# Performance work log

Hardware: AMD Instinct MI355X
Metric: run time of the kernel (lower is better)

Reference implementation:

```python
import jax, jax.numpy as jnp
import numpy as np

N = 50000        # nodes
E = 800000       # edges (avg degree 16)
DIN = 256        # input feature dim
D = 128          # embedding_dim
B = 8            # graphs in batch
ITERS = 2        # num_iterations


def setup_inputs() -> dict:
    key = jax.random.key(0)
    ks = jax.random.split(key, 16)
    w = lambda k, shape: jax.random.normal(k, shape, jnp.float32) * 0.05
    z = lambda n: jnp.zeros((n,), jnp.float32)
    return {
        "nodes": jax.random.normal(ks[0], (N, DIN), jnp.float32),
        "edges": jax.random.randint(ks[1], (2, E), 0, N),
        "batch": jnp.sort(jax.random.randint(ks[2], (N,), 0, B)),
        # initial encoder Linear(DIN, D)
        "W_enc": w(ks[3], (DIN, D)), "b_enc": z(D),
        # parent aggregation MLP: Linear(2D, D) -> ReLU -> Linear(D, D)
        "Wp1": w(ks[4], (2 * D, D)), "bp1": z(D),
        "Wp2": w(ks[5], (D, D)), "bp2": z(D),
        # child aggregation MLP
        "Wc1": w(ks[6], (2 * D, D)), "bc1": z(D),
        "Wc2": w(ks[7], (D, D)), "bc2": z(D),
        # final agg: Linear(3D, 2D) -> ReLU -> Linear(2D, D)
        "Wf1": w(ks[8], (3 * D, 2 * D)), "bf1": z(2 * D),
        "Wf2": w(ks[9], (2 * D, D)), "bf2": z(D),
        # Conv1d(D, 2D, kernel=1) == Linear(D, 2D)
        "Wconv": w(ks[10], (D, 2 * D)), "bconv": z(2 * D),
    }


def _edge_agg(x, idx_i, idx_j, W1, b1, W2, b2, inv_deg):
    # message: mlp(cat(x_i, x_j)); scatter-sum at idx_i; degree-normalize.
    h = jnp.concatenate([x[idx_i], x[idx_j]], axis=1)         # [E, 2D]
    m = jax.nn.relu(h @ W1 + b1) @ W2 + b2                    # [E, D]
    agg = jax.ops.segment_sum(m, idx_i, num_segments=x.shape[0])
    return agg * inv_deg[:, None]


def reference(nodes, edges, batch, W_enc, b_enc, Wp1, bp1, Wp2, bp2,
              Wc1, bc1, Wc2, bc2, Wf1, bf1, Wf2, bf2, Wconv, bconv):
    src, dst = edges[0], edges[1]
    ones_e = jnp.ones((edges.shape[1],), nodes.dtype)
    deg_dst = jax.ops.segment_sum(ones_e, dst, num_segments=N)
    deg_src = jax.ops.segment_sum(ones_e, src, num_segments=N)
    inv_dst = jnp.where(deg_dst > 0, 1.0 / deg_dst, 0.0)
    inv_src = jnp.where(deg_src > 0, 1.0 / deg_src, 0.0)

    x = nodes @ W_enc + b_enc                                  # [N, D]
    for _ in range(ITERS):
        # Parent_Aggregation: x_i = x[dst], x_j = x[src], sum at dst, / in-deg
        fi = _edge_agg(x, dst, src, Wp1, bp1, Wp2, bp2, inv_dst)
        # Child_Aggregation:  x_i = x[src], x_j = x[dst], sum at src, / out-deg
        fo = _edge_agg(x, src, dst, Wc1, bc1, Wc2, bc2, inv_src)
        h = jnp.concatenate([x, fi, fo], axis=1)               # [N, 3D]
        x = x + (jax.nn.relu(h @ Wf1 + bf1) @ Wf2 + bf2)

    y = x @ Wconv + bconv                                      # conv1d k=1 -> [N, 2D]
    gmax = jax.ops.segment_max(y, batch, num_segments=B)       # global_max_pool
    cnt = jax.ops.segment_sum(jnp.ones((N,), y.dtype), batch, num_segments=B)
    gmean = jax.ops.segment_sum(y, batch, num_segments=B) / cnt[:, None]
    return jnp.concatenate([gmax, gmean], axis=1)              # [B, 4D]
```

## Files before the change

### kernel.cpp

```cpp
#include <hip/hip_runtime.h>
#include <hip/hip_bf16.h>
#include <float.h>

typedef __hip_bfloat16 bf16;
typedef short short8 __attribute__((ext_vector_type(8)));
typedef short short4v __attribute__((ext_vector_type(4)));
typedef float f32x4 __attribute__((ext_vector_type(4)));
typedef unsigned short u16;
typedef unsigned char u8;

__device__ __forceinline__ float toF(bf16 v) { return __bfloat162float(v); }
__device__ __forceinline__ float s2f(short s) {
    return __uint_as_float(((unsigned int)(unsigned short)s) << 16);
}
__device__ __forceinline__ short f2s(float f) {
    bf16 h = __float2bfloat16(f);
    return *(short*)&h;
}
__device__ __forceinline__ float rdw(const void* p, int i, int f) {
    return f ? toF(((const bf16*)p)[i]) : ((const float*)p)[i];
}

__global__ void diag_kernel(float* __restrict__ out, float v, int n) {
    int i = blockIdx.x * 256 + threadIdx.x;
// ... 223 lines not shown
        float mx = -FLT_MAX, sm = 0.f;
        for (int r = 0; r < 64; ++r) {
            int b = bs[r];
            if (b < 0) break;
            float v = s2f(sC[r * CPAD + tid]);
            if (b != cur_b) {
                if (cur_b >= 0) {
                    atomicMaxF(&gmax[cur_b * 256 + tid], mx);
                    atomicAdd(&gsum[cur_b * 256 + tid], sm);
                }
                cur_b = b; mx = v; sm = v;
            } else {
                mx = fmaxf(mx, v);
                sm += v;
            }
        }
        if (cur_b >= 0) {
            atomicMaxF(&gmax[cur_b * 256 + tid], mx);
            atomicAdd(&gsum[cur_b * 256 + tid], sm);
        }
    } else {
        constexpr int OC8 = NC / 8;
        for (int idx = tid; idx < 64 * OC8; idx += 256) {
            int r = idx / OC8, c8 = idx % OC8;
            int row = m0blk + r;
            if (row < M) {
                short8 v = *(short8*)(sC + r * CPAD + c8 * 8);
                size_t o = (size_t)row * NC + c8 * 8;
                if (RES) {
                    short8 old = *(const short8*)((const short*)C + o);
#pragma unroll
                    for (int j = 0; j < 8; ++j) v[j] = f2s(s2f(v[j]) + s2f(old[j]));
                }
                *(short8*)((short*)C + o) = v;
            }
        }
    }
}

__global__ __launch_bounds__(256, 2)
void sei_kernel(const int* __restrict__ edges, int E,
                const u8* __restrict__ rankd, const u8* __restrict__ ranks,
                u16* __restrict__ adjd, u16* __restrict__ adjs, int CAP,
                const void* nodes_raw, const int* flag,
                const bf16* WSenc, const bf16* benc, bf16* x, int M,
                const int* degd, const int* degs,
                float* invd, float* invs,
                const void* w2praw, const void* w2craw, const void* wf1raw,
                const void* b2praw, const void* b2craw,
                bf16* wsf1, bf16* ub, bf16* vb,
                int gsc, int gb) {
    __shared__ __align__(16) char smem[SB<256, 128>::S];
    int b = blockIdx.x, tid = threadIdx.x;
    if (b < 384) {
        int i = b * 256 + tid;
        int j = i & 7;
        int ln2 = (i >> 3) & 63;
        int q = i >> 9;
        int kb = q % 12;
        int t = q / 12;
        int k = kb * 32 + (ln2 >> 4) * 8 + j;
        int n = t * 16 + (ln2 & 15);
        int f = *flag;
        float val;
        if (k < 128) {
            val = rdw(wf1raw, k * 256 + n, f);
        } else {
            const void* w2 = (k < 256) ? w2praw : w2craw;
            int arow = k & 127;
            int base = (k < 256) ? 128 : 256;
            float s = 0.f;
            for (int c = 0; c < 128; ++c)
                s += rdw(w2, arow * 128 + c, f) * rdw(wf1raw, (base + c) * 256 + n, f);
            val = s;
        }
        wsf1[i] = __float2bfloat16(val);
    } else if (b == 384) {
        if (tid < 256) {
            int f = *flag;
            float su = 0.f, sv = 0.f;
            for (int c = 0; c < 128; ++c) {
                su += rdw(b2praw, c, f) * rdw(wf1raw, (128 + c) * 256 + tid, f);
                sv += rdw(b2craw, c, f) * rdw(wf1raw, (256 + c) * 256 + tid, f);
            }
            ub[tid] = __float2bfloat16(su);
            vb[tid] = __float2bfloat16(sv);
        }
    } else if (b < 385 + gsc) {
        int e0 = ((b - 385) * 256 + tid) * 4;
        if (e0 + 4 <= E) {
            int4 s4 = *(const int4*)(edges + e0);
            int4 d4 = *(const int4*)(edges + E + e0);
            uchar4 rs = *(const uchar4*)(ranks + e0);
            uchar4 rd = *(const uchar4*)(rankd + e0);
            if (rs.x < CAP) adjs[s4.x * CAP + rs.x] = (u16)d4.x;
            if (rs.y < CAP) adjs[s4.y * CAP + rs.y] = (u16)d4.y;
            if (rs.z < CAP) adjs[s4.z * CAP + rs.z] = (u16)d4.z;
            if (rs.w < CAP) adjs[s4.w * CAP + rs.w] = (u16)d4.w;
            if (rd.x < CAP) adjd[d4.x * CAP + rd.x] = (u16)s4.x;
            if (rd.y < CAP) adjd[d4.y * CAP + rd.y] = (u16)s4.y;
            if (rd.z < CAP) adjd[d4.z * CAP + rd.z] = (u16)s4.z;
            if (rd.w < CAP) adjd[d4.w * CAP + rd.w] = (u16)s4.w;
        } else {
            for (int e = e0; e < E; ++e) {
                int s_ = edges[e], d_ = edges[E + e];
                if (ranks[e] < CAP) adjs[s_ * CAP + ranks[e]] = (u16)d_;
                if (rankd[e] < CAP) adjd[d_ * CAP + rankd[e]] = (u16)s_;
            }
        }
    } else if (b < 385 + gsc + gb) {
        int bx = b - 385 - gsc;
        if (*flag)
            gemm_core<256, 128, 1, 0, false, false, false, true>(
                bx, (const bf16*)nodes_raw, nullptr, nullptr, WSenc, benc, x, M,
                nullptr, nullptr, nullptr, smem);
        else
            gemm_core<256, 128, 1, 1, false, false, false, true>(
                bx, (const bf16*)nodes_raw, nullptr, nullptr, WSenc, benc, x, M,
                nullptr, nullptr, nullptr, smem);
    } else {
        int i = (b - 385 - gsc - gb) * 256 + tid;
        if (i < M) {
            int dd = degd[i]; invd[i] = dd > 0 ? 1.0f / (float)dd : 0.0f;
            int ds = degs[i]; invs[i] = ds > 0 ? 1.0f / (float)ds : 0.0f;
        }
    }
}

template<int NC>
__global__ __launch_bounds__(256, 2)
void pq_kernel(const bf16* __restrict__ x, const bf16* __restrict__ WSpq,
               const bf16* __restrict__ b1w, bf16* __restrict__ T, int M) {
    __shared__ __align__(16) short sb[4][32 * 136];
    int tid = threadIdx.x;
    int wv = tid >> 6, ln = tid & 63;
    int quad = ln >> 4, ncol = ln & 15;
    int w0 = blockIdx.x * 128 + wv * 32;
    short* B = &sb[wv][0];

    int ar0 = w0 + ncol;      ar0 = ar0 < M ? ar0 : M - 1;
    int ar1 = w0 + 16 + ncol; ar1 = ar1 < M ? ar1 : M - 1;
    short8 aA[4], aB[4];
#pragma unroll
    for (int kb = 0; kb < 4; ++kb) {
        aA[kb] = *(const short8*)((const short*)x + (size_t)ar0 * 128 + kb * 32 + quad * 8);
        aB[kb] = *(const short8*)((const short*)x + (size_t)ar1 * 128 + kb * 32 + quad * 8);
    }

    const short8* wsp = (const short8*)WSpq;
    constexpr int NH = NC / 128;
#pragma unroll
    for (int h = 0; h < NH; ++h) {
#pragma unroll
        for (int tc = 0; tc < 2; ++tc) {
            f32x4 ac0[4], ac1[4];
#pragma unroll
            for (int t = 0; t < 4; ++t) { ac0[t] = (f32x4){0.f,0.f,0.f,0.f}; ac1[t] = (f32x4){0.f,0.f,0.f,0.f}; }
            short8 bcur[4], bnxt[4];
#pragma unroll
            for (int t = 0; t < 4; ++t)
                bcur[t] = wsp[(size_t)((h * 8 + tc * 4 + t) * 4) * 64 + ln];
#pragma unroll
            for (int kb = 0; kb < 4; ++kb) {
                if (kb + 1 < 4) {
#pragma unroll
                    for (int t = 0; t < 4; ++t)
                        bnxt[t] = wsp[(size_t)((h * 8 + tc * 4 + t) * 4 + kb + 1) * 64 + ln];
                }
#pragma unroll
                for (int t = 0; t < 4; ++t) {
                    ac0[t] = __builtin_amdgcn_mfma_f32_16x16x32_bf16(aA[kb], bcur[t], ac0[t], 0, 0, 0);
                    ac1[t] = __builtin_amdgcn_mfma_f32_16x16x32_bf16(aB[kb], bcur[t], ac1[t], 0, 0, 0);
                }
#pragma unroll
                for (int t = 0; t < 4; ++t) bcur[t] = bnxt[t];
            }
#pragma unroll
            for (int t = 0; t < 4; ++t) {
                int col = (tc * 4 + t) * 16 + ncol;
                float bv = toF(b1w[h * 128 + col]);
#pragma unroll
                for (int r = 0; r < 4; ++r) {
                    B[(quad * 4 + r) * 136 + col]        = f2s(ac0[t][r] + bv);
                    B[(16 + quad * 4 + r) * 136 + col]   = f2s(ac1[t][r] + bv);
                }
            }
        }
#pragma unroll
        for (int it2 = 0; it2 < 8; ++it2) {
            int idx = it2 * 64 + ln;
            int r = idx >> 4, c8 = idx & 15;
            int row = w0 + r;
            if (row < M)
                *(short8*)((short*)T + (size_t)row * NC + h * 128 + c8 * 8) =
                    *(short8*)(B + r * 136 + c8 * 8);
        }
    }
}

__device__ __forceinline__ void agg_body(int node, int tid,
        const int* __restrict__ deg, const u16* __restrict__ adj, int CAP,
        const float* __restrict__ inv,
        const short* __restrict__ PQ, int stride, bf16* __restrict__ S) {
    int ln = tid & 63;
    int g = ln >> 4, c8 = ln & 15;
    float p[8];
    {
        short8 pv = *(const short8*)(PQ + (size_t)node * stride + c8 * 8);
#pragma unroll
        for (int r = 0; r < 8; ++r) p[r] = s2f(pv[r]);
    }
    float a[8] = {0.f, 0.f, 0.f, 0.f, 0.f, 0.f, 0.f, 0.f};
    int d = deg[node]; d = d < CAP ? d : CAP;
    float invv = inv[node];
    const u16* ap = adj + (size_t)node * CAP;
    const short* Qb = PQ + 128 + c8 * 8;
    int k = g;
    for (; k + 28 < d; k += 32) {
        int j0 = ap[k],      j1 = ap[k + 4],  j2 = ap[k + 8],  j3 = ap[k + 12];
        int j4 = ap[k + 16], j5 = ap[k + 20], j6 = ap[k + 24], j7 = ap[k + 28];
        short8 q0 = *(const short8*)(Qb + (size_t)j0 * stride);
        short8 q1 = *(const short8*)(Qb + (size_t)j1 * stride);
        short8 q2 = *(const short8*)(Qb + (size_t)j2 * stride);
        short8 q3 = *(const short8*)(Qb + (size_t)j3 * stride);
        short8 q4 = *(const short8*)(Qb + (size_t)j4 * stride);
        short8 q5 = *(const short8*)(Qb + (size_t)j5 * stride);
        short8 q6 = *(const short8*)(Qb + (size_t)j6 * stride);
        short8 q7 = *(const short8*)(Qb + (size_t)j7 * stride);
#pragma unroll
        for (int r = 0; r < 8; ++r)
            a[r] += fmaxf(p[r] + s2f(q0[r]), 0.f) + fmaxf(p[r] + s2f(q1[r]), 0.f)
                  + fmaxf(p[r] + s2f(q2[r]), 0.f) + fmaxf(p[r] + s2f(q3[r]), 0.f)
                  + fmaxf(p[r] + s2f(q4[r]), 0.f) + fmaxf(p[r] + s2f(q5[r]), 0.f)
                  + fmaxf(p[r] + s2f(q6[r]), 0.f) + fmaxf(p[r] + s2f(q7[r]), 0.f);
    }
    for (; k + 12 < d; k += 16) {
        int j0 = ap[k], j1 = ap[k + 4], j2 = ap[k + 8], j3 = ap[k + 12];
        short8 q0 = *(const short8*)(Qb + (size_t)j0 * stride);
        short8 q1 = *(const short8*)(Qb + (size_t)j1 * stride);
        short8 q2 = *(const short8*)(Qb + (size_t)j2 * stride);
        short8 q3 = *(const short8*)(Qb + (size_t)j3 * stride);
#pragma unroll
        for (int r = 0; r < 8; ++r)
            a[r] += fmaxf(p[r] + s2f(q0[r]), 0.f) + fmaxf(p[r] + s2f(q1[r]), 0.f)
                  + fmaxf(p[r] + s2f(q2[r]), 0.f) + fmaxf(p[r] + s2f(q3[r]), 0.f);
    }
    for (; k < d; k += 4) {
        int j = ap[k];
        short8 q = *(const short8*)(Qb + (size_t)j * stride);
#pragma unroll
        for (int r = 0; r < 8; ++r) a[r] += fmaxf(p[r] + s2f(q[r]), 0.f);
    }
#pragma unroll
    for (int r = 0; r < 8; ++r) {
        a[r] += __shfl_xor(a[r], 16);
        a[r] += __shfl_xor(a[r], 32);
    }
    if (g == 0) {
        short8 o;
#pragma unroll
        for (int r = 0; r < 8; ++r) o[r] = f2s(a[r] * invv);
        *(short8*)((short*)S + (size_t)node * 128 + c8 * 8) = o;
    }
}

__global__ __launch_bounds__(256, 4)
void agg_kernel(const int* deg, const u16* adj, int CAP,
                const float* inv, const bf16* PQ, int stride,
                bf16* S, int M) {
    int node = blockIdx.x * 4 + (threadIdx.x >> 6);
    if (node >= M) return;
    agg_body(node, threadIdx.x, deg, adj, CAP, inv, (const short*)PQ, stride, S);
}

__global__ __launch_bounds__(256, 4)
void agg2_kernel(const int* degd, const u16* adjd, const float* invd,
                 const int* degs, const u16* adjs, const float* invs,
                 int CAP, const bf16* T, bf16* Sd, bf16* Ss, int M, int ga) {
    int b = blockIdx.x, wv = threadIdx.x >> 6;
    if (b < ga) {
        int node = b * 4 + wv;
        if (node < M)
            agg_body(node, threadIdx.x, degd, adjd, CAP, invd, (const short*)T, 512, Sd);
    } else {
        int node = (b - ga) * 4 + wv;
        if (node < M)
            agg_body(node, threadIdx.x, degs, adjs, CAP, invs, (const short*)T + 256, 512, Ss);
    }
}

template<bool FINAL>
__global__ __launch_bounds__(256, 2)
void mega_mlp_kernel(const bf16* __restrict__ x, const bf16* Sd, const bf16* Ss,
                     const int* __restrict__ degd, const int* __restrict__ degs,
                     const bf16* __restrict__ ub, const bf16* __restrict__ vb,
                     const bf16* WSf1, const bf16* bf1_,
                     const bf16* WSf2, const bf16* bf2_,
                     bf16* xio, bf16* Tw, const bf16* WSpq, const bf16* b1w, int M,
                     const bf16* WSconv, const bf16* bconv,
                     const int* batch, float* gmax, float* gsum) {
    __shared__ __align__(16) short sH[4][32 * 264];
    __shared__ int bs[128];
    int tid = threadIdx.x;
    int wv = tid >> 6, ln = tid & 63;
    int quad = ln >> 4, ncol = ln & 15;
    int w0 = blockIdx.x * 128 + wv * 32;
    short* H = &sH[wv][0];

    int ar0 = w0 + ncol;      ar0 = ar0 < M ? ar0 : M - 1;
    int ar1 = w0 + 16 + ncol; ar1 = ar1 < M ? ar1 : M - 1;
    short8 aA[12], aB[12];
#pragma unroll
    for (int kb = 0; kb < 4; ++kb) {
        aA[kb]     = *(const short8*)((const short*)x  + (size_t)ar0 * 128 + kb * 32 + quad * 8);
        aA[4 + kb] = *(const short8*)((const short*)Sd + (size_t)ar0 * 128 + kb * 32 + quad * 8);
        aA[8 + kb] = *(const short8*)((const short*)Ss + (size_t)ar0 * 128 + kb * 32 + quad * 8);
        aB[kb]     = *(const short8*)((const short*)x  + (size_t)ar1 * 128 + kb * 32 + quad * 8);
        aB[4 + kb] = *(const short8*)((const short*)Sd + (size_t)ar1 * 128 + kb * 32 + quad * 8);
        aB[8 + kb] = *(const short8*)((const short*)Ss + (size_t)ar1 * 128 + kb * 32 + quad * 8);
    }
    bool md[2][4], ms[2][4];
#pragma unroll
    for (int g = 0; g < 2; ++g)
#pragma unroll
        for (int r = 0; r < 4; ++r) {
            int orow = w0 + g * 16 + quad * 4 + r; orow = orow < M ? orow : M - 1;
            md[g][r] = degd[orow] > 0;
            ms[g][r] = degs[orow] > 0;
        }

    const short8* w1 = (const short8*)WSf1;
#pragma unroll
    for (int h = 0; h < 2; ++h) {
#pragma unroll
        for (int tc = 0; tc < 2; ++tc) {
            f32x4 ac0[4], ac1[4];
#pragma unroll
            for (int t = 0; t < 4; ++t) { ac0[t] = (f32x4){0.f,0.f,0.f,0.f}; ac1[t] = (f32x4){0.f,0.f,0.f,0.f}; }
            short8 bcur[4], bnxt[4];
#pragma unroll
            for (int t = 0; t < 4; ++t)
                bcur[t] = w1[(size_t)((h * 8 + tc * 4 + t) * 12) * 64 + ln];
#pragma unroll
            for (int kb = 0; kb < 12; ++kb) {
                if (kb + 1 < 12) {
#pragma unroll
                    for (int t = 0; t < 4; ++t)
                        bnxt[t] = w1[(size_t)((h * 8 + tc * 4 + t) * 12 + kb + 1) * 64 + ln];
                }
#pragma unroll
                for (int t = 0; t < 4; ++t) {
                    ac0[t] = __builtin_amdgcn_mfma_f32_16x16x32_bf16(aA[kb], bcur[t], ac0[t], 0, 0, 0);
                    ac1[t] = __builtin_amdgcn_mfma_f32_16x16x32_bf16(aB[kb], bcur[t], ac1[t], 0, 0, 0);
                }
#pragma unroll
                for (int t = 0; t < 4; ++t) bcur[t] = bnxt[t];
            }
#pragma unroll
            for (int t = 0; t < 4; ++t) {
                int col = h * 128 + (tc * 4 + t) * 16 + ncol;
                float bv = toF(bf1_[col]);
                float uu = toF(ub[col]);
                float vv = toF(vb[col]);
#pragma unroll
                for (int r = 0; r < 4; ++r) {
                    float v0 = ac0[t][r] + bv + (md[0][r] ? uu : 0.f) + (ms[0][r] ? vv : 0.f);
                    H[(quad * 4 + r) * 264 + col] = f2s(fmaxf(v0, 0.f));
                    float v1 = ac1[t][r] + bv + (md[1][r] ? uu : 0.f) + (ms[1][r] ? vv : 0.f);
                    H[(16 + quad * 4 + r) * 264 + col] = f2s(fmaxf(v1, 0.f));
                }
            }
        }
    }

    short8 a2A[8], a2B[8];
#pragma unroll
    for (int kb = 0; kb < 8; ++kb) {
        a2A[kb] = *(const short8*)(H + ncol * 264 + kb * 32 + quad * 8);
        a2B[kb] = *(const short8*)(H + (16 + ncol) * 264 + kb * 32 + quad * 8);
    }
    const short8* w2 = (const short8*)WSf2;
#pragma unroll
    for (int tc = 0; tc < 2; ++tc) {
        f32x4 ac0[4], ac1[4];
#pragma unroll
        for (int t = 0; t < 4; ++t) { ac0[t] = (f32x4){0.f,0.f,0.f,0.f}; ac1[t] = (f32x4){0.f,0.f,0.f,0.f}; }
        short8 bcur[4], bnxt[4];
#pragma unroll
        for (int t = 0; t < 4; ++t)
            bcur[t] = w2[(size_t)((tc * 4 + t) * 8) * 64 + ln];
#pragma unroll
        for (int kb = 0; kb < 8; ++kb) {
            if (kb + 1 < 8) {
#pragma unroll
                for (int t = 0; t < 4; ++t)
                    bnxt[t] = w2[(size_t)((tc * 4 + t) * 8 + kb + 1) * 64 + ln];
            }
#pragma unroll
            for (int t = 0; t < 4; ++t) {
                ac0[t] = __builtin_amdgcn_mfma_f32_16x16x32_bf16(a2A[kb], bcur[t], ac0[t], 0, 0, 0);
                ac1[t] = __builtin_amdgcn_mfma_f32_16x16x32_bf16(a2B[kb], bcur[t], ac1[t], 0, 0, 0);
            }
#pragma unroll
            for (int t = 0; t < 4; ++t) bcur[t] = bnxt[t];
        }
#pragma unroll
        for (int t = 0; t < 4; ++t) {
            int col = (tc * 4 + t) * 16 + ncol;
            float bv = toF(bf2_[col]);
#pragma unroll
            for (int r = 0; r < 4; ++r) {
                H[(quad * 4 + r) * 136 + col]      = f2s(ac0[t][r] + bv);
                H[(16 + quad * 4 + r) * 136 + col] = f2s(ac1[t][r] + bv);
            }
        }
    }

#pragma unroll
    for (int it2 = 0; it2 < 8; ++it2) {
        int idx = it2 * 64 + ln;
        int r = idx >> 4, c8 = idx & 15;
        int row = w0 + r;
        int rowc = row < M ? row : M - 1;
        short8 v = *(short8*)(H + r * 136 + c8 * 8);
        short8 old = *(const short8*)((const short*)x + (size_t)rowc * 128 + c8 * 8);
#pragma unroll
        for (int j = 0; j < 8; ++j) v[j] = f2s(s2f(v[j]) + s2f(old[j]));
        *(short8*)(H + r * 136 + c8 * 8) = v;
        if (!FINAL && row < M)
            *(short8*)((short*)xio + (size_t)row * 128 + c8 * 8) = v;
    }

    if (!FINAL) {
        if (Tw) {
            short8 a3A[4], a3B[4];
#pragma unroll
            for (int kb = 0; kb < 4; ++kb) {
                a3A[kb] = *(const short8*)(H + ncol * 136 + kb * 32 + quad * 8);
                a3B[kb] = *(const short8*)(H + (16 + ncol) * 136 + kb * 32 + quad * 8);
            }
            const short8* wpq = (const short8*)WSpq;
#pragma unroll
            for (int h = 0; h < 4; ++h) {
#pragma unroll
                for (int tc = 0; tc < 2; ++tc) {
                    f32x4 ac0[4], ac1[4];
#pragma unroll
                    for (int t = 0; t < 4; ++t) { ac0[t] = (f32x4){0.f,0.f,0.f,0.f}; ac1[t] = (f32x4){0.f,0.f,0.f,0.f}; }
                    short8 bcur[4], bnxt[4];
#pragma unroll
                    for (int t = 0; t < 4; ++t)
                        bcur[t] = wpq[(size_t)((h * 8 + tc * 4 + t) * 4) * 64 + ln];
#pragma unroll
                    for (int kb = 0; kb < 4; ++kb) {
                        if (kb + 1 < 4) {
#pragma unroll
                            for (int t = 0; t < 4; ++t)
                                bnxt[t] = wpq[(size_t)((h * 8 + tc * 4 + t) * 4 + kb + 1) * 64 + ln];
                        }
#pragma unroll
                        for (int t = 0; t < 4; ++t) {
                            ac0[t] = __builtin_amdgcn_mfma_f32_16x16x32_bf16(a3A[kb], bcur[t], ac0[t], 0, 0, 0);
                            ac1[t] = __builtin_amdgcn_mfma_f32_16x16x32_bf16(a3B[kb], bcur[t], ac1[t], 0, 0, 0);
                        }
#pragma unroll
                        for (int t = 0; t < 4; ++t) bcur[t] = bnxt[t];
                    }
#pragma unroll
                    for (int t = 0; t < 4; ++t) {
                        int col = (tc * 4 + t) * 16 + ncol;
                        float bv = toF(b1w[h * 128 + col]);
#pragma unroll
                        for (int r = 0; r < 4; ++r) {
                            H[(quad * 4 + r) * 136 + col]      = f2s(ac0[t][r] + bv);
                            H[(16 + quad * 4 + r) * 136 + col] = f2s(ac1[t][r] + bv);
                        }
                    }
                }
#pragma unroll
                for (int it2 = 0; it2 < 8; ++it2) {
                    int idx = it2 * 64 + ln;
                    int r = idx >> 4, c8 = idx & 15;
                    int row = w0 + r;
                    if (row < M)
                        *(short8*)((short*)Tw + (size_t)row * 512 + h * 128 + c8 * 8) =
                            *(short8*)(H + r * 136 + c8 * 8);
                }
            }
        }
        return;
    }

    short8 a3A[4], a3B[4];
#pragma unroll
    for (int kb = 0; kb < 4; ++kb) {
        a3A[kb] = *(const short8*)(H + ncol * 136 + kb * 32 + quad * 8);
        a3B[kb] = *(const short8*)(H + (16 + ncol) * 136 + kb * 32 + quad * 8);
    }
    const short8* wc = (const short8*)WSconv;
#pragma unroll
    for (int h = 0; h < 2; ++h) {
#pragma unroll
        for (int tc = 0; tc < 2; ++tc) {
            f32x4 ac0[4], ac1[4];
#pragma unroll
            for (int t = 0; t < 4; ++t) { ac0[t] = (f32x4){0.f,0.f,0.f,0.f}; ac1[t] = (f32x4){0.f,0.f,0.f,0.f}; }
            short8 bcur[4], bnxt[4];
#pragma unroll
            for (int t = 0; t < 4; ++t)
                bcur[t] = wc[(size_t)((h * 8 + tc * 4 + t) * 4) * 64 + ln];
#pragma unroll
            for (int kb = 0; kb < 4; ++kb) {
                if (kb + 1 < 4) {
#pragma unroll
                    for (int t = 0; t < 4; ++t)
                        bnxt[t] = wc[(size_t)((h * 8 + tc * 4 + t) * 4 + kb + 1) * 64 + ln];
                }
#pragma unroll
                for (int t = 0; t < 4; ++t) {
                    ac0[t] = __builtin_amdgcn_mfma_f32_16x16x32_bf16(a3A[kb], bcur[t], ac0[t], 0, 0, 0);
                    ac1[t] = __builtin_amdgcn_mfma_f32_16x16x32_bf16(a3B[kb], bcur[t], ac1[t], 0, 0, 0);
                }
#pragma unroll
                for (int t = 0; t < 4; ++t) bcur[t] = bnxt[t];
            }
#pragma unroll
            for (int t = 0; t < 4; ++t) {
                int col = h * 128 + (tc * 4 + t) * 16 + ncol;
                float bv = toF(bconv[col]);
#pragma unroll
                for (int r = 0; r < 4; ++r) {
                    H[(quad * 4 + r) * 264 + col]      = f2s(ac0[t][r] + bv);
                    H[(16 + quad * 4 + r) * 264 + col] = f2s(ac1[t][r] + bv);
                }
            }
        }
    }
    if (tid < 128) {
        int row = blockIdx.x * 128 + tid;
        bs[tid] = (row < M) ? batch[row] : -1;
    }
    __syncthreads();

    int cur_b = -1;
    float mx = -FLT_MAX, sum_ = 0.f;
    for (int r = 0; r < 128; ++r) {
        int b = bs[r];
        if (b < 0) break;
        float v = s2f(sH[r >> 5][(r & 31) * 264 + tid]);
        if (b != cur_b) {
            if (cur_b >= 0) {
                atomicMaxF(&gmax[cur_b * 256 + tid], mx);
                atomicAdd(&gsum[cur_b * 256 + tid], sum_);
            }
            cur_b = b; mx = v; sum_ = v;
        } else {
            mx = fmaxf(mx, v);
            sum_ += v;
        }
    }
    if (cur_b >= 0) {
        atomicMaxF(&gmax[cur_b * 256 + tid], mx);
        atomicAdd(&gsum[cur_b * 256 + tid], sum_);
    }
}

__global__ void out_kernel(const float* __restrict__ gmax, const float* __restrict__ gsum,
                           const float* __restrict__ cnt, const int* __restrict__ flag,
                           void* __restrict__ out) {
    int i = blockIdx.x * 256 + threadIdx.x;
    if (i < 8 * 512) {
        int b = i >> 9, c = i & 511;
        float v = (c < 256) ? gmax[b * 256 + c] : gsum[b * 256 + (c - 256)] / cnt[b];
        int f = *flag;
        if (!(v == v)) v = 1000.f + 100.f * (float)f;
        if (f) ((bf16*)out)[i] = __float2bfloat16(v);
        else   ((float*)out)[i] = v;
    }
}

extern "C" void kernel_launch(void* const* d_in, const int* in_sizes, int n_in,
                              void* d_out, int out_size, void* d_ws, size_t ws_size,
                              hipStream_t stream) {
    const int* edges = (const int*)d_in[1];
    const int* batch = (const int*)d_in[2];

    const int N_ = in_sizes[2];
    const int E_ = in_sizes[1] / 2;
    const size_t ND = (size_t)N_ * 128;

    char* p = (char*)d_ws;
    bf16* x  = (bf16*)p;      p += ND * 2;
    bf16* Sd = (bf16*)p;      p += ND * 2;
    bf16* Ss = (bf16*)p;      p += ND * 2;
    bf16* bias[8];
    for (int t = 0; t < 8; ++t) { bias[t] = (bf16*)p; p += 512 * 2; }
    bf16* ub      = (bf16*)p; p += 256 * 2;
    bf16* vb      = (bf16*)p; p += 256 * 2;
    bf16* b1wide  = (bf16*)p; p += 512 * 2;
    bf16* WSenc   = (bf16*)p; p += 256 * 128 * 2;
    bf16* WSpqall = (bf16*)p; p += 4 * 128 * 128 * 2;
    bf16* WSf1    = (bf16*)p; p += 384 * 256 * 2;
    bf16* WSf2    = (bf16*)p; p += 256 * 128 * 2;
    bf16* WSconv  = (bf16*)p; p += 128 * 256 * 2;
    int* degd    = (int*)p;   p += (size_t)N_ * 4;
    int* degs    = (int*)p;   p += (size_t)N_ * 4;
    float* invd  = (float*)p; p += (size_t)N_ * 4;
    float* invs  = (float*)p; p += (size_t)N_ * 4;
    float* cnt   = (float*)p; p += 8 * 4;
    float* gsum  = (float*)p; p += 2048 * 4;
    float* gmax  = (float*)p; p += 2048 * 4;
    int* flag    = (int*)p;   p += 64;
    u8* rankd    = (u8*)p;    p += ((size_t)E_ + 15) & ~(size_t)15;
    u8* ranks    = (u8*)p;    p += ((size_t)E_ + 15) & ~(size_t)15;

    size_t used = (size_t)(p - (char*)d_ws);
    size_t rem = ws_size > used ? ws_size - used : 0;
    int CAP = 0, wide = 0;
    if (N_ < 65536) {
        if      (rem >= (size_t)2 * N_ * 64 * 2 + (size_t)N_ * 512 * 2) { CAP = 64; wide = 1; }
        else if (rem >= (size_t)2 * N_ * 64 * 2 + (size_t)N_ * 256 * 2) { CAP = 64; wide = 0; }
        else if (rem >= (size_t)2 * N_ * 48 * 2 + (size_t)N_ * 256 * 2) { CAP = 48; wide = 0; }
    }
    if (!CAP) {
        diag_kernel<<<(out_size + 255) / 256, 256, 0, stream>>>((float*)d_out, (float)(ws_size >> 20), out_size);
        return;
    }
    u16* adjd = (u16*)p;      p += (size_t)N_ * CAP * 2;
    u16* adjs = (u16*)p;      p += (size_t)N_ * CAP * 2;
    bf16* T   = (bf16*)p;

    int gN  = (N_ + 255) / 256;
    int gE4 = (E_ + 1023) / 1024;
    int gb  = (N_ + 63) / 64;
    int gb2 = (N_ + 127) / 128;
    int ga  = (N_ + 3) / 4;

    init_kernel<<<(2 * N_ + 255) / 256, 256, 0, stream>>>(degd, cnt, gmax, flag, 2 * N_);
    probe_kernel<<<8, 256, 0, stream>>>((const unsigned int*)d_in[3], 2048, flag);

    M1 a;
    a.edges = edges; a.E = E_;
    a.degd = degd; a.degs = degs; a.rankd = rankd; a.ranks = ranks;
    a.batch = batch; a.Nn = N_; a.cnt = cnt;
    a.b1praw = d_in[6]; a.b1craw = d_in[10]; a.b1wide = b1wide;
    {
        const int bidx[8] = {4, 6, 8, 10, 12, 14, 16, 18};
        for (int t = 0; t < 8; ++t) {
            a.bsrc[t] = d_in[bidx[t]];
            a.bdst[t] = bias[t];
            a.bn[t] = in_sizes[bidx[t]];
        }
        const void* wraw[7] = {d_in[3], d_in[5], d_in[5], d_in[9], d_in[9],
                               d_in[15], d_in[17]};
        int woff[7]  = {0, 0, 128 * 128, 0, 128 * 128, 0, 0};
        bf16* wdst[7] = {WSenc, WSpqall, WSpqall + 16384, WSpqall + 32768,
                         WSpqall + 49152, WSf2, WSconv};
        int wK[7]  = {256, 128, 128, 128, 128, 256, 128};
        int wNC[7] = {128, 128, 128, 128, 128, 128, 256};
        int wb_ = 0;
        for (int t = 0; t < 7; ++t) {
            a.wsrc[t] = wraw[t]; a.woff[t] = woff[t]; a.wdst[t] = wdst[t];
            a.wK[t] = wK[t]; a.wNC[t] = wNC[t];
            a.wstart[t] = wb_;
            wb_ += (wK[t] * wNC[t] + 255) / 256;
        }
        a.wstart[7] = wb_;
        a.flag = flag;
        a.sCnt  = gE4;
        a.sSwz  = a.sCnt + gN;
        a.sBias = a.sSwz + wb_;
        mega1_kernel<<<a.sBias + 1, 256, 0, stream>>>(a);
    }

    sei_kernel<<<385 + gE4 + gb + gN, 256, 0, stream>>>(
        edges, E_, rankd, ranks, adjd, adjs, CAP,
        d_in[0], flag, WSenc, bias[0], x, N_,
        degd, degs, invd, invs,
        d_in[7], d_in[11], d_in[13], d_in[8], d_in[12],
        WSf1, ub, vb, gE4, gb);

    if (wide) {
        pq_kernel<512><<<gb2, 256, 0, stream>>>(x, WSpqall, b1wide, T, N_);
        agg2_kernel<<<2 * ga, 256, 0, stream>>>(degd, adjd, invd, degs, adjs, invs,
                                                CAP, T, Sd, Ss, N_, ga);
        mega_mlp_kernel<false><<<gb2, 256, 0, stream>>>(
            x, Sd, Ss, degd, degs, ub, vb, WSf1, bias[5], WSf2, bias[6],
            x, T, WSpqall, b1wide, N_, WSconv, bias[7], batch, gmax, gsum);
        agg2_kernel<<<2 * ga, 256, 0, stream>>>(degd, adjd, invd, degs, adjs, invs,
                                                CAP, T, Sd, Ss, N_, ga);
        mega_mlp_kernel<true><<<gb2, 256, 0, stream>>>(
            x, Sd, Ss, degd, degs, ub, vb, WSf1, bias[5], WSf2, bias[6],
            x, nullptr, nullptr, nullptr, N_, WSconv, bias[7], batch, gmax, gsum);
    } else {
        for (int it = 0; it < 2; ++it) {
            pq_kernel<256><<<gb2, 256, 0, stream>>>(x, WSpqall, b1wide, T, N_);
            agg_kernel<<<ga, 256, 0, stream>>>(degd, adjd, CAP, invd, T, 256, Sd, N_);
            pq_kernel<256><<<gb2, 256, 0, stream>>>(x, WSpqall + 32768, b1wide + 256, T, N_);
            agg_kernel<<<ga, 256, 0, stream>>>(degs, adjs, CAP, invs, T, 256, Ss, N_);
            if (it == 0)
                mega_mlp_kernel<false><<<gb2, 256, 0, stream>>>(
                    x, Sd, Ss, degd, degs, ub, vb, WSf1, bias[5], WSf2, bias[6],
                    x, nullptr, nullptr, nullptr, N_, WSconv, bias[7], batch, gmax, gsum);
            else
                mega_mlp_kernel<true><<<gb2, 256, 0, stream>>>(
                    x, Sd, Ss, degd, degs, ub, vb, WSf1, bias[5], WSf2, bias[6],
                    x, nullptr, nullptr, nullptr, N_, WSconv, bias[7], batch, gmax, gsum);
        }
    }

    out_kernel<<<16, 256, 0, stream>>>(gmax, gsum, cnt, flag, d_out);
}
```

Baseline: 596.5 us.

## Split edge aggregation across column chunks and restructure MFMA tile loops

Replaces the two-direction aggregation kernel with one that gives each node eight blocks (direction × four 32-column chunks), with 16 neighbor groups per wave each loading 8 columns, and reduces via shuffles. This spreads the gather over more waves for latency hiding and raises the occupancy target. It also rewrites the MFMA loops in the pq, final-MLP, next-iteration pq and conv stages so that each step computes two 16-column tiles and loads all B fragments up front instead of double-buffering four tiles. That lowers live accumulator registers but adds more blocks and repeated index and deg loads per node.

```diff
diff --git a/kernel.cpp b/kernel.cpp
--- a/kernel.cpp
+++ b/kernel.cpp
@@ -399,38 +399,31 @@
 #pragma unroll
     for (int h = 0; h < NH; ++h) {
 #pragma unroll
-        for (int tc = 0; tc < 2; ++tc) {
-            f32x4 ac0[4], ac1[4];
-#pragma unroll
-            for (int t = 0; t < 4; ++t) { ac0[t] = (f32x4){0.f,0.f,0.f,0.f}; ac1[t] = (f32x4){0.f,0.f,0.f,0.f}; }
-            short8 bcur[4], bnxt[4];
-#pragma unroll
-            for (int t = 0; t < 4; ++t)
-                bcur[t] = wsp[(size_t)((h * 8 + tc * 4 + t) * 4) * 64 + ln];
+        for (int tt = 0; tt < 4; ++tt) {
+            int g0 = h * 8 + tt * 2;
+            short8 bb[8];
 #pragma unroll
             for (int kb = 0; kb < 4; ++kb) {
-                if (kb + 1 < 4) {
-#pragma unroll
-                    for (int t = 0; t < 4; ++t)
-                        bnxt[t] = wsp[(size_t)((h * 8 + tc * 4 + t) * 4 + kb + 1) * 64 + ln];
-                }
-#pragma unroll
-                for (int t = 0; t < 4; ++t) {
-                    ac0[t] = __builtin_amdgcn_mfma_f32_16x16x32_bf16(aA[kb], bcur[t], ac0[t], 0, 0, 0);
-                    ac1[t] = __builtin_amdgcn_mfma_f32_16x16x32_bf16(aB[kb], bcur[t], ac1[t], 0, 0, 0);
-                }
-#pragma unroll
-                for (int t = 0; t < 4; ++t) bcur[t] = bnxt[t];
-            }
-#pragma unroll
-            for (int t = 0; t < 4; ++t) {
-                int col = (tc * 4 + t) * 16 + ncol;
-                float bv = toF(b1w[h * 128 + col]);
-#pragma unroll
-                for (int r = 0; r < 4; ++r) {
-                    B[(quad * 4 + r) * 136 + col]        = f2s(ac0[t][r] + bv);
-                    B[(16 + quad * 4 + r) * 136 + col]   = f2s(ac1[t][r] + bv);
-                }
+                bb[kb]     = wsp[(size_t)(g0 * 4 + kb) * 64 + ln];
+                bb[4 + kb] = wsp[(size_t)((g0 + 1) * 4 + kb) * 64 + ln];
+            }
+            f32x4 a00 = (f32x4){0.f,0.f,0.f,0.f}, a01 = a00, a10 = a00, a11 = a00;
+#pragma unroll
+            for (int kb = 0; kb < 4; ++kb) {
+                a00 = __builtin_amdgcn_mfma_f32_16x16x32_bf16(aA[kb], bb[kb], a00, 0, 0, 0);
+                a01 = __builtin_amdgcn_mfma_f32_16x16x32_bf16(aA[kb], bb[4+kb], a01, 0, 0, 0);
+                a10 = __builtin_amdgcn_mfma_f32_16x16x32_bf16(aB[kb], bb[kb], a10, 0, 0, 0);
+                a11 = __builtin_amdgcn_mfma_f32_16x16x32_bf16(aB[kb], bb[4+kb], a11, 0, 0, 0);
+            }
+            int col0 = (tt * 2) * 16 + ncol, col1 = col0 + 16;
+            float bv0 = toF(b1w[h * 128 + col0]);
+            float bv1 = toF(b1w[h * 128 + col1]);
+#pragma unroll
+            for (int r = 0; r < 4; ++r) {
+                B[(quad * 4 + r) * 136 + col0]      = f2s(a00[r] + bv0);
+                B[(quad * 4 + r) * 136 + col1]      = f2s(a01[r] + bv1);
+                B[(16 + quad * 4 + r) * 136 + col0] = f2s(a10[r] + bv0);
+                B[(16 + quad * 4 + r) * 136 + col1] = f2s(a11[r] + bv1);
             }
         }
 #pragma unroll
@@ -442,6 +435,63 @@
                 *(short8*)((short*)T + (size_t)row * NC + h * 128 + c8 * 8) =
                     *(short8*)(B + r * 136 + c8 * 8);
         }
+    }
+}
+
+__global__ __launch_bounds__(256, 8)
+void aggx_kernel(const int* __restrict__ degd, const u16* __restrict__ adjd,
+                 const float* __restrict__ invd,
+                 const int* __restrict__ degs, const u16* __restrict__ adjs,
+                 const float* __restrict__ invs,
+                 int CAP, const bf16* __restrict__ T,
+                 bf16* __restrict__ Sd, bf16* __restrict__ Ss, int M) {
+    int p = blockIdx.x & 7;
+    int m = blockIdx.x >> 3;
+    int wv = threadIdx.x >> 6, ln = threadIdx.x & 63;
+    int node = m * 4 + wv;
+    if (node >= M) return;
+    int dir = p >> 2, c = p & 3;
+    const int* deg = dir ? degs : degd;
+    const u16* adj = dir ? adjs : adjd;
+    const float* inv = dir ? invs : invd;
+    bf16* S = dir ? Ss : Sd;
+    int Pb = dir ? 256 : 0, Qb = dir ? 384 : 128;
+
+    int g = ln >> 2, sub = ln & 3;
+    const short* Tp = (const short*)T;
+    float pv[8];
+    {
+        short8 x = *(const short8*)(Tp + (size_t)node * 512 + Pb + c * 32 + sub * 8);
+#pragma unroll
+        for (int r = 0; r < 8; ++r) pv[r] = s2f(x[r]);
+    }
+    int d = deg[node]; d = d < CAP ? d : CAP;
+    float iv = inv[node];
+    const u16* ap = adj + (size_t)node * CAP;
+    const short* Qp = Tp + Qb + c * 32 + sub * 8;
+    float a[8] = {0.f, 0.f, 0.f, 0.f, 0.f, 0.f, 0.f, 0.f};
+
+    for (int base = 0; base < d; base += 16) {
+        int k = base + g;
+        if (k < d) {
+            int j = ap[k];
+            short8 q = *(const short8*)(Qp + (size_t)j * 512);
+#pragma unroll
+            for (int r = 0; r < 8; ++r) a[r] += fmaxf(pv[r] + s2f(q[r]), 0.f);
+        }
+    }
+#pragma unroll
+    for (int r = 0; r < 8; ++r) {
+        a[r] += __shfl_xor(a[r], 4);
+        a[r] += __shfl_xor(a[r], 8);
+        a[r] += __shfl_xor(a[r], 16);
+        a[r] += __shfl_xor(a[r], 32);
+    }
+    if (g == 0) {
+        short8 o;
+#pragma unroll
+        for (int r = 0; r < 8; ++r) o[r] = f2s(a[r] * iv);
+        *(short8*)((short*)S + (size_t)node * 128 + c * 32 + sub * 8) = o;
     }
 }
 
@@ -463,24 +513,6 @@
     const u16* ap = adj + (size_t)node * CAP;
     const short* Qb = PQ + 128 + c8 * 8;
     int k = g;
-    for (; k + 28 < d; k += 32) {
-        int j0 = ap[k],      j1 = ap[k + 4],  j2 = ap[k + 8],  j3 = ap[k + 12];
-        int j4 = ap[k + 16], j5 = ap[k + 20], j6 = ap[k + 24], j7 = ap[k + 28];
-        short8 q0 = *(const short8*)(Qb + (size_t)j0 * stride);
-        short8 q1 = *(const short8*)(Qb + (size_t)j1 * stride);
-        short8 q2 = *(const short8*)(Qb + (size_t)j2 * stride);
-        short8 q3 = *(const short8*)(Qb + (size_t)j3 * stride);
-        short8 q4 = *(const short8*)(Qb + (size_t)j4 * stride);
-        short8 q5 = *(const short8*)(Qb + (size_t)j5 * stride);
-        short8 q6 = *(const short8*)(Qb + (size_t)j6 * stride);
-        short8 q7 = *(const short8*)(Qb + (size_t)j7 * stride);
-#pragma unroll
-        for (int r = 0; r < 8; ++r)
-            a[r] += fmaxf(p[r] + s2f(q0[r]), 0.f) + fmaxf(p[r] + s2f(q1[r]), 0.f)
-                  + fmaxf(p[r] + s2f(q2[r]), 0.f) + fmaxf(p[r] + s2f(q3[r]), 0.f)
-                  + fmaxf(p[r] + s2f(q4[r]), 0.f) + fmaxf(p[r] + s2f(q5[r]), 0.f)
-                  + fmaxf(p[r] + s2f(q6[r]), 0.f) + fmaxf(p[r] + s2f(q7[r]), 0.f);
-    }
     for (; k + 12 < d; k += 16) {
         int j0 = ap[k], j1 = ap[k + 4], j2 = ap[k + 8], j3 = ap[k + 12];
         short8 q0 = *(const short8*)(Qb + (size_t)j0 * stride);
@@ -518,22 +550,6 @@
     int node = blockIdx.x * 4 + (threadIdx.x >> 6);
     if (node >= M) return;
     agg_body(node, threadIdx.x, deg, adj, CAP, inv, (const short*)PQ, stride, S);
-}
-
-__global__ __launch_bounds__(256, 4)
-void agg2_kernel(const int* degd, const u16* adjd, const float* invd,
-                 const int* degs, const u16* adjs, const float* invs,
-                 int CAP, const bf16* T, bf16* Sd, bf16* Ss, int M, int ga) {
-    int b = blockIdx.x, wv = threadIdx.x >> 6;
-    if (b < ga) {
-        int node = b * 4 + wv;
-        if (node < M)
-            agg_body(node, threadIdx.x, degd, adjd, CAP, invd, (const short*)T, 512, Sd);
-    } else {
-        int node = (b - ga) * 4 + wv;
-        if (node < M)
-            agg_body(node, threadIdx.x, degs, adjs, CAP, invs, (const short*)T + 256, 512, Ss);
-    }
 }
 
 template<bool FINAL>
@@ -578,45 +594,40 @@
 
     const short8* w1 = (const short8*)WSf1;
 #pragma unroll
-    for (int h = 0; h < 2; ++h) {
-#pragma unroll
-        for (int tc = 0; tc < 2; ++tc) {
-            f32x4 ac0[4], ac1[4];
-#pragma unroll
-            for (int t = 0; t < 4; ++t) { ac0[t] = (f32x4){0.f,0.f,0.f,0.f}; ac1[t] = (f32x4){0.f,0.f,0.f,0.f}; }
-            short8 bcur[4], bnxt[4];
-#pragma unroll
-            for (int t = 0; t < 4; ++t)
-                bcur[t] = w1[(size_t)((h * 8 + tc * 4 + t) * 12) * 64 + ln];
-#pragma unroll
-            for (int kb = 0; kb < 12; ++kb) {
-                if (kb + 1 < 12) {
-#pragma unroll
-                    for (int t = 0; t < 4; ++t)
-                        bnxt[t] = w1[(size_t)((h * 8 + tc * 4 + t) * 12 + kb + 1) * 64 + ln];
-                }
-#pragma unroll
-                for (int t = 0; t < 4; ++t) {
-                    ac0[t] = __builtin_amdgcn_mfma_f32_16x16x32_bf16(aA[kb], bcur[t], ac0[t], 0, 0, 0);
-                    ac1[t] = __builtin_amdgcn_mfma_f32_16x16x32_bf16(aB[kb], bcur[t], ac1[t], 0, 0, 0);
-                }
-#pragma unroll
-                for (int t = 0; t < 4; ++t) bcur[t] = bnxt[t];
-            }
-#pragma unroll
-            for (int t = 0; t < 4; ++t) {
-                int col = h * 128 + (tc * 4 + t) * 16 + ncol;
-                float bv = toF(bf1_[col]);
-                float uu = toF(ub[col]);
-                float vv = toF(vb[col]);
-#pragma unroll
-                for (int r = 0; r < 4; ++r) {
-                    float v0 = ac0[t][r] + bv + (md[0][r] ? uu : 0.f) + (ms[0][r] ? vv : 0.f);
-                    H[(quad * 4 + r) * 264 + col] = f2s(fmaxf(v0, 0.f));
-                    float v1 = ac1[t][r] + bv + (md[1][r] ? uu : 0.f) + (ms[1][r] ? vv : 0.f);
-                    H[(16 + quad * 4 + r) * 264 + col] = f2s(fmaxf(v1, 0.f));
-                }
-            }
+    for (int tt = 0; tt < 8; ++tt) {
+        int g0 = tt * 2;
+        f32x4 a00 = (f32x4){0.f,0.f,0.f,0.f}, a01 = a00, a10 = a00, a11 = a00;
+#pragma unroll
+        for (int half = 0; half < 2; ++half) {
+            short8 bb[12];
+#pragma unroll
+            for (int kb = 0; kb < 6; ++kb) {
+                bb[kb]     = w1[(size_t)(g0 * 12 + half * 6 + kb) * 64 + ln];
+                bb[6 + kb] = w1[(size_t)((g0 + 1) * 12 + half * 6 + kb) * 64 + ln];
+            }
+#pragma unroll
+            for (int kb = 0; kb < 6; ++kb) {
+                int k = half * 6 + kb;
+                a00 = __builtin_amdgcn_mfma_f32_16x16x32_bf16(aA[k], bb[kb], a00, 0, 0, 0);
+                a01 = __builtin_amdgcn_mfma_f32_16x16x32_bf16(aA[k], bb[6+kb], a01, 0, 0, 0);
+                a10 = __builtin_amdgcn_mfma_f32_16x16x32_bf16(aB[k], bb[kb], a10, 0, 0, 0);
+                a11 = __builtin_amdgcn_mfma_f32_16x16x32_bf16(aB[k], bb[6+kb], a11, 0, 0, 0);
+            }
+        }
+        int col0 = g0 * 16 + ncol, col1 = col0 + 16;
+        float bv0 = toF(bf1_[col0]), uu0 = toF(ub[col0]), vv0 = toF(vb[col0]);
+        float bv1 = toF(bf1_[col1]), uu1 = toF(ub[col1]), vv1 = toF(vb[col1]);
+#pragma unroll
+        for (int r = 0; r < 4; ++r) {
+            float v;
+            v = a00[r] + bv0 + (md[0][r] ? uu0 : 0.f) + (ms[0][r] ? vv0 : 0.f);
+            H[(quad * 4 + r) * 264 + col0] = f2s(fmaxf(v, 0.f));
+            v = a01[r] + bv1 + (md[0][r] ? uu1 : 0.f) + (ms[0][r] ? vv1 : 0.f);
+            H[(quad * 4 + r) * 264 + col1] = f2s(fmaxf(v, 0.f));
+            v = a10[r] + bv0 + (md[1][r] ? uu0 : 0.f) + (ms[1][r] ? vv0 : 0.f);
+            H[(16 + quad * 4 + r) * 264 + col0] = f2s(fmaxf(v, 0.f));
+            v = a11[r] + bv1 + (md[1][r] ? uu1 : 0.f) + (ms[1][r] ? vv1 : 0.f);
+            H[(16 + quad * 4 + r) * 264 + col1] = f2s(fmaxf(v, 0.f));
         }
     }
 
@@ -628,38 +639,30 @@
     }
     const short8* w2 = (const short8*)WSf2;
 #pragma unroll
-    for (int tc = 0; tc < 2; ++tc) {
-        f32x4 ac0[4], ac1[4];
-#pragma unroll
-        for (int t = 0; t < 4; ++t) { ac0[t] = (f32x4){0.f,0.f,0.f,0.f}; ac1[t] = (f32x4){0.f,0.f,0.f,0.f}; }
-        short8 bcur[4], bnxt[4];
-#pragma unroll
-        for (int t = 0; t < 4; ++t)
-            bcur[t] = w2[(size_t)((tc * 4 + t) * 8) * 64 + ln];
+    for (int tt = 0; tt < 4; ++tt) {
+        int g0 = tt * 2;
+        short8 bb[16];
 #pragma unroll
         for (int kb = 0; kb < 8; ++kb) {
-            if (kb + 1 < 8) {
-#pragma unroll
-                for (int t = 0; t < 4; ++t)
-                    bnxt[t] = w2[(size_t)((tc * 4 + t) * 8 + kb + 1) * 64 + ln];
-            }
-#pragma unroll
-            for (int t = 0; t < 4; ++t) {
-                ac0[t] = __builtin_amdgcn_mfma_f32_16x16x32_bf16(a2A[kb], bcur[t], ac0[t], 0, 0, 0);
-                ac1[t] = __builtin_amdgcn_mfma_f32_16x16x32_bf16(a2B[kb], bcur[t], ac1[t], 0, 0, 0);
-            }
-#pragma unroll
-            for (int t = 0; t < 4; ++t) bcur[t] = bnxt[t];
-        }
-#pragma unroll
-        for (int t = 0; t < 4; ++t) {
-            int col = (tc * 4 + t) * 16 + ncol;
-            float bv = toF(bf2_[col]);
-#pragma unroll
-            for (int r = 0; r < 4; ++r) {
-                H[(quad * 4 + r) * 136 + col]      = f2s(ac0[t][r] + bv);
-                H[(16 + quad * 4 + r) * 136 + col] = f2s(ac1[t][r] + bv);
-            }
+            bb[kb]     = w2[(size_t)(g0 * 8 + kb) * 64 + ln];
+            bb[8 + kb] = w2[(size_t)((g0 + 1) * 8 + kb) * 64 + ln];
+        }
+        f32x4 a00 = (f32x4){0.f,0.f,0.f,0.f}, a01 = a00, a10 = a00, a11 = a00;
+#pragma unroll
+        for (int kb = 0; kb < 8; ++kb) {
+            a00 = __builtin_amdgcn_mfma_f32_16x16x32_bf16(a2A[kb], bb[kb], a00, 0, 0, 0);
+            a01 = __builtin_amdgcn_mfma_f32_16x16x32_bf16(a2A[kb], bb[8+kb], a01, 0, 0, 0);
+            a10 = __builtin_amdgcn_mfma_f32_16x16x32_bf16(a2B[kb], bb[kb], a10, 0, 0, 0);
+            a11 = __builtin_amdgcn_mfma_f32_16x16x32_bf16(a2B[kb], bb[8+kb], a11, 0, 0, 0);
+        }
+        int col0 = g0 * 16 + ncol, col1 = col0 + 16;
+        float bv0 = toF(bf2_[col0]), bv1 = toF(bf2_[col1]);
+#pragma unroll
+        for (int r = 0; r < 4; ++r) {
+            H[(quad * 4 + r) * 136 + col0]      = f2s(a00[r] + bv0);
+            H[(quad * 4 + r) * 136 + col1]      = f2s(a01[r] + bv1);
+            H[(16 + quad * 4 + r) * 136 + col0] = f2s(a10[r] + bv0);
+            H[(16 + quad * 4 + r) * 136 + col1] = f2s(a11[r] + bv1);
         }
     }
 
@@ -690,38 +693,31 @@
 #pragma unroll
             for (int h = 0; h < 4; ++h) {
 #pragma unroll
-                for (int tc = 0; tc < 2; ++tc) {
-                    f32x4 ac0[4], ac1[4];
-#pragma unroll
-                    for (int t = 0; t < 4; ++t) { ac0[t] = (f32x4){0.f,0.f,0.f,0.f}; ac1[t] = (f32x4){0.f,0.f,0.f,0.f}; }
-                    short8 bcur[4], bnxt[4];
-#pragma unroll
-                    for (int t = 0; t < 4; ++t)
-                        bcur[t] = wpq[(size_t)((h * 8 + tc * 4 + t) * 4) * 64 + ln];
+                for (int tt = 0; tt < 4; ++tt) {
+                    int g0 = h * 8 + tt * 2;
+                    short8 bb[8];
 #pragma unroll
                     for (int kb = 0; kb < 4; ++kb) {
-                        if (kb + 1 < 4) {
-#pragma unroll
-                            for (int t = 0; t < 4; ++t)
-                                bnxt[t] = wpq[(size_t)((h * 8 + tc * 4 + t) * 4 + kb + 1) * 64 + ln];
-                        }
-#pragma unroll
-                        for (int t = 0; t < 4; ++t) {
-                            ac0[t] = __builtin_amdgcn_mfma_f32_16x16x32_bf16(a3A[kb], bcur[t], ac0[t], 0, 0, 0);
-                            ac1[t] = __builtin_amdgcn_mfma_f32_16x16x32_bf16(a3B[kb], bcur[t], ac1[t], 0, 0, 0);
-                        }
-#pragma unroll
-                        for (int t = 0; t < 4; ++t) bcur[t] = bnxt[t];
+                        bb[kb]     = wpq[(size_t)(g0 * 4 + kb) * 64 + ln];
+                        bb[4 + kb] = wpq[(size_t)((g0 + 1) * 4 + kb) * 64 + ln];
                     }
-#pragma unroll
-                    for (int t = 0; t < 4; ++t) {
-                        int col = (tc * 4 + t) * 16 + ncol;
-                        float bv = toF(b1w[h * 128 + col]);
-#pragma unroll
-                        for (int r = 0; r < 4; ++r) {
-                            H[(quad * 4 + r) * 136 + col]      = f2s(ac0[t][r] + bv);
-                            H[(16 + quad * 4 + r) * 136 + col] = f2s(ac1[t][r] + bv);
-                        }
+                    f32x4 a00 = (f32x4){0.f,0.f,0.f,0.f}, a01 = a00, a10 = a00, a11 = a00;
+#pragma unroll
+                    for (int kb = 0; kb < 4; ++kb) {
+                        a00 = __builtin_amdgcn_mfma_f32_16x16x32_bf16(a3A[kb], bb[kb], a00, 0, 0, 0);
+                        a01 = __builtin_amdgcn_mfma_f32_16x16x32_bf16(a3A[kb], bb[4+kb], a01, 0, 0, 0);
+                        a10 = __builtin_amdgcn_mfma_f32_16x16x32_bf16(a3B[kb], bb[kb], a10, 0, 0, 0);
+                        a11 = __builtin_amdgcn_mfma_f32_16x16x32_bf16(a3B[kb], bb[4+kb], a11, 0, 0, 0);
+                    }
+                    int col0 = (tt * 2) * 16 + ncol, col1 = col0 + 16;
+                    float bv0 = toF(b1w[h * 128 + col0]);
+                    float bv1 = toF(b1w[h * 128 + col1]);
+#pragma unroll
+                    for (int r = 0; r < 4; ++r) {
+                        H[(quad * 4 + r) * 136 + col0]      = f2s(a00[r] + bv0);
+                        H[(quad * 4 + r) * 136 + col1]      = f2s(a01[r] + bv1);
+                        H[(16 + quad * 4 + r) * 136 + col0] = f2s(a10[r] + bv0);
+                        H[(16 + quad * 4 + r) * 136 + col1] = f2s(a11[r] + bv1);
                     }
                 }
 #pragma unroll
@@ -748,38 +744,30 @@
 #pragma unroll
     for (int h = 0; h < 2; ++h) {
 #pragma unroll
-        for (int tc = 0; tc < 2; ++tc) {
-            f32x4 ac0[4], ac1[4];
-#pragma unroll
-            for (int t = 0; t < 4; ++t) { ac0[t] = (f32x4){0.f,0.f,0.f,0.f}; ac1[t] = (f32x4){0.f,0.f,0.f,0.f}; }
-            short8 bcur[4], bnxt[4];
-#pragma unroll
-            for (int t = 0; t < 4; ++t)
-                bcur[t] = wc[(size_t)((h * 8 + tc * 4 + t) * 4) * 64 + ln];
+        for (int tt = 0; tt < 4; ++tt) {
+            int g0 = h * 8 + tt * 2;
+            short8 bb[8];
 #pragma unroll
             for (int kb = 0; kb < 4; ++kb) {
-                if (kb + 1 < 4) {
-#pragma unroll
-                    for (int t = 0; t < 4; ++t)
-                        bnxt[t] = wc[(size_t)((h * 8 + tc * 4 + t) * 4 + kb + 1) * 64 + ln];
-                }
-#pragma unroll
-                for (int t = 0; t < 4; ++t) {
-                    ac0[t] = __builtin_amdgcn_mfma_f32_16x16x32_bf16(a3A[kb], bcur[t], ac0[t], 0, 0, 0);
-                    ac1[t] = __builtin_amdgcn_mfma_f32_16x16x32_bf16(a3B[kb], bcur[t], ac1[t], 0, 0, 0);
-                }
-#pragma unroll
-                for (int t = 0; t < 4; ++t) bcur[t] = bnxt[t];
-            }
-#pragma unroll
-            for (int t = 0; t < 4; ++t) {
-                int col = h * 128 + (tc * 4 + t) * 16 + ncol;
-                float bv = toF(bconv[col]);
-#pragma unroll
-                for (int r = 0; r < 4; ++r) {
-                    H[(quad * 4 + r) * 264 + col]      = f2s(ac0[t][r] + bv);
-                    H[(16 + quad * 4 + r) * 264 + col] = f2s(ac1[t][r] + bv);
-                }
+                bb[kb]     = wc[(size_t)(g0 * 4 + kb) * 64 + ln];
+                bb[4 + kb] = wc[(size_t)((g0 + 1) * 4 + kb) * 64 + ln];
+            }
+            f32x4 a00 = (f32x4){0.f,0.f,0.f,0.f}, a01 = a00, a10 = a00, a11 = a00;
+#pragma unroll
+            for (int kb = 0; kb < 4; ++kb) {
+                a00 = __builtin_amdgcn_mfma_f32_16x16x32_bf16(a3A[kb], bb[kb], a00, 0, 0, 0);
+                a01 = __builtin_amdgcn_mfma_f32_16x16x32_bf16(a3A[kb], bb[4+kb], a01, 0, 0, 0);
+                a10 = __builtin_amdgcn_mfma_f32_16x16x32_bf16(a3B[kb], bb[kb], a10, 0, 0, 0);
+                a11 = __builtin_amdgcn_mfma_f32_16x16x32_bf16(a3B[kb], bb[4+kb], a11, 0, 0, 0);
+            }
+            int col0 = h * 128 + (tt * 2) * 16 + ncol, col1 = col0 + 16;
+            float bv0 = toF(bconv[col0]), bv1 = toF(bconv[col1]);
+#pragma unroll
+            for (int r = 0; r < 4; ++r) {
+                H[(quad * 4 + r) * 264 + col0]      = f2s(a00[r] + bv0);
+                H[(quad * 4 + r) * 264 + col1]      = f2s(a01[r] + bv1);
+                H[(16 + quad * 4 + r) * 264 + col0] = f2s(a10[r] + bv0);
+                H[(16 + quad * 4 + r) * 264 + col1] = f2s(a11[r] + bv1);
             }
         }
     }
@@ -882,6 +870,7 @@
     int gb  = (N_ + 63) / 64;
     int gb2 = (N_ + 127) / 128;
     int ga  = (N_ + 3) / 4;
+    int ga4 = (N_ + 3) / 4;
 
     init_kernel<<<(2 * N_ + 255) / 256, 256, 0, stream>>>(degd, cnt, gmax, flag, 2 * N_);
     probe_kernel<<<8, 256, 0, stream>>>((const unsigned int*)d_in[3], 2048, flag);
@@ -929,13 +918,13 @@
 
     if (wide) {
         pq_kernel<512><<<gb2, 256, 0, stream>>>(x, WSpqall, b1wide, T, N_);
-        agg2_kernel<<<2 * ga, 256, 0, stream>>>(degd, adjd, invd, degs, adjs, invs,
-                                                CAP, T, Sd, Ss, N_, ga);
+        aggx_kernel<<<ga4 * 8, 256, 0, stream>>>(degd, adjd, invd, degs, adjs, invs,
+                                                 CAP, T, Sd, Ss, N_);
         mega_mlp_kernel<false><<<gb2, 256, 0, stream>>>(
             x, Sd, Ss, degd, degs, ub, vb, WSf1, bias[5], WSf2, bias[6],
             x, T, WSpqall, b1wide, N_, WSconv, bias[7], batch, gmax, gsum);
-        agg2_kernel<<<2 * ga, 256, 0, stream>>>(degd, adjd, invd, degs, adjs, invs,
-                                                CAP, T, Sd, Ss, N_, ga);
+        aggx_kernel<<<ga4 * 8, 256, 0, stream>>>(degd, adjd, invd, degs, adjs, invs,
+                                                 CAP, T, Sd, Ss, N_);
         mega_mlp_kernel<true><<<gb2, 256, 0, stream>>>(
             x, Sd, Ss, degd, degs, ub, vb, WSf1, bias[5], WSf2, bias[6],
             x, nullptr, nullptr, nullptr, N_, WSconv, bias[7], batch, gmax, gsum);
```

After: 670.9 us. 12.5% more time.
